# Performance work log

Measured on AMD Instinct MI355X. Metric: run time of the kernel, lower is better.

## Reference

```python
import jax, jax.numpy as jnp
import numpy as np

D_MODEL = 1024
H = 16
D_HEAD = D_MODEL // H
MASK_VAL = -1e30


def setup_inputs() -> dict:
    key = jax.random.key(0)
    ks = jax.random.split(key, 10)
    B, S = 2, 2048
    scale = 1.0 / np.sqrt(D_MODEL)
    return {
        "query": jax.random.normal(ks[0], (B, S, D_MODEL), jnp.float32),
        "key": jax.random.normal(ks[1], (B, S, D_MODEL), jnp.float32),
        "value": jax.random.normal(ks[2], (B, S, D_MODEL), jnp.float32),
        "mask": jax.random.randint(ks[3], (B, S, S), 0, 2) > 0,
        "Wq": jax.random.normal(ks[4], (D_MODEL, D_MODEL), jnp.float32) * scale,
        "bq": jnp.zeros((D_MODEL,), jnp.float32),
        "Wk": jax.random.normal(ks[5], (D_MODEL, D_MODEL), jnp.float32) * scale,
        "bk": jnp.zeros((D_MODEL,), jnp.float32),
        "Wv": jax.random.normal(ks[6], (D_MODEL, D_MODEL), jnp.float32) * scale,
        "bv": jnp.zeros((D_MODEL,), jnp.float32),
    }


def _split_heads(x, B, S):
    # [B,S,D] -> [B,H,S,Dh]
    return x.reshape(B, S, H, D_HEAD).transpose(0, 2, 1, 3)


def reference(query, key, value, mask, Wq, bq, Wk, bk, Wv, bv):
    B, S, _ = query.shape
    q = _split_heads(query @ Wq.T + bq, B, S)
    k = _split_heads(key @ Wk.T + bk, B, S)
    v = _split_heads(value @ Wv.T + bv, B, S)
    # scale by sqrt of per-head dim (query.size(-1) after split)
    q = q / jnp.sqrt(jnp.asarray(D_HEAD, q.dtype))
    scores = jnp.einsum("bhqd,bhkd->bhqk", q, k)
    scores = jnp.where(mask[:, None, :, :], MASK_VAL, scores)
    attn = jax.nn.softmax(scores, axis=-1)
    out = jnp.einsum("bhqk,bhkd->bhqd", attn, v)
    return out.transpose(0, 2, 1, 3).reshape(B, S, D_MODEL)
```

## Files before the change

kernel.cpp:

```cpp
#include <hip/hip_runtime.h>
#include <hip/hip_bf16.h>

#define D_MODEL 1024
#define NH 16
#define DH 64
#define S_LEN 2048
#define BATCH 2
#define QSCALE (0.125f * 1.44269504088896f)

#define KV_HSTRIDE (S_LEN * DH)
#define WS_V_OFF   (NH * KV_HSTRIDE)
#define KVB_WORDS  (2 * NH * KV_HSTRIDE)
#define MB_WORDS   ((S_LEN / 64) * S_LEN)
#define KTILE 128
#define NT (S_LEN / KTILE)
#define X_ELEMS (BATCH * S_LEN * D_MODEL)
#define W_ELEMS (D_MODEL * D_MODEL)
#define KSTR 88
#define VSTR 136
#define BUFW (128 * KSTR + 64 * VSTR)
#define BUF_BYTES (BUFW * 2)

typedef __attribute__((ext_vector_type(8))) short bf16x8;
typedef __attribute__((ext_vector_type(4))) float f32x4;
typedef __attribute__((ext_vector_type(2))) unsigned int u32x2;

static __device__ inline unsigned short f2bf(float f) {
    union { float f; unsigned u; } v; v.f = f;
    unsigned r = v.u + 0x7fffu + ((v.u >> 16) & 1u);
    return (unsigned short)(r >> 16);
}
static __device__ inline unsigned cvt2(float a, float b) {
    union { __hip_bfloat162 h2; unsigned u; } cv;
    cv.h2 = __float22bfloat162_rn(make_float2(a, b));
    return cv.u;
}
static __device__ inline bf16x8 pack8(f32x4 a, f32x4 b) {
    union { bf16x8 v; unsigned u[4]; } r;
    r.u[0] = cvt2(a[0], a[1]); r.u[1] = cvt2(a[2], a[3]);
    r.u[2] = cvt2(b[0], b[1]); r.u[3] = cvt2(b[2], b[3]);
    return r.v;
}
static __device__ inline bf16x8 cvt8(const float* __restrict__ p) {
    return pack8(*(const f32x4*)p, *(const f32x4*)(p + 4));
}
static __device__ inline float exp2_fast(float x) {
#if __has_builtin(__builtin_amdgcn_exp2f)
    return __builtin_amdgcn_exp2f(x);
#else
    return exp2f(x);
#endif
}
static __device__ inline void gload_lds16(const unsigned short* __restrict__ g,
                                          unsigned short* l, int lane) {
#if __has_builtin(__builtin_amdgcn_global_load_lds)
    __builtin_amdgcn_global_load_lds(
        (const __attribute__((address_space(1))) void*)g,
        (__attribute__((address_space(3))) void*)l, 16, 0, 0);
#else
    *(bf16x8*)((char*)l + lane * 16) = *(const bf16x8*)g;
#endif
}
static __device__ inline int vperm(int s) {
    return (s & ~31) | ((s & 12) << 1) | ((s & 16) >> 2) | (s & 3);
}

__global__ __launch_bounds__(256) void cvt_kernel(
    const float* __restrict__ q, const float* __restrict__ k,
    const float* __restrict__ v,
    const float* __restrict__ Wq, const float* __restrict__ Wk,
    const float* __restrict__ Wv,
    unsigned short* __restrict__ xb, unsigned short* __restrict__ wb)
{
    const int by = blockIdx.y;
    const float* src;
    unsigned short* dst;
    size_t base;
    if (blockIdx.x < 1024) {
        src = by == 0 ? q : (by == 1 ? k : v);
        dst = xb + (size_t)by * X_ELEMS;
        base = (size_t)blockIdx.x * 4096;
    } else {
        src = by == 0 ? Wq : (by == 1 ? Wk : Wv);
        dst = wb + (size_t)by * W_ELEMS;
        base = (size_t)(blockIdx.x - 1024) * 4096;
    }
    const int tid = threadIdx.x;
#pragma unroll
    for (int j = 0; j < 4; ++j) {
        const size_t o = base + (size_t)j * 1024 + (size_t)tid * 4;
        const f32x4 a = *(const f32x4*)(src + o);
        u32x2 r;
        r[0] = cvt2(a[0], a[1]);
        r[1] = cvt2(a[2], a[3]);
        *(u32x2*)&dst[o] = r;
    }
}

__global__ __launch_bounds__(256) void pack_mask_kernel(
    const int* __restrict__ mask, unsigned long long* __restrict__ mbits,
    int b_base)
{
    const int w    = blockIdx.x * 4 + (threadIdx.x >> 6);
    const int lane = threadIdx.x & 63;
    const int b    = b_base + (w >> 16);
    const int rem  = w & 65535;
    const int kt   = rem >> 11;
    const int s    = rem & 2047;
    const int v = mask[((size_t)b * S_LEN + s) * S_LEN + kt * 64 + lane];
    const unsigned long long bits = __ballot(v != 0);
    if (lane == 0) mbits[w] = bits;
}

__global__ __launch_bounds__(256) void proj_v2_kernel(
    const unsigned short* __restrict__ xb, const unsigned short* __restrict__ wb,
    const float* __restrict__ bq, const float* __restrict__ bk,
    const float* __restrict__ bv,
    float* __restrict__ q_out, unsigned short* __restrict__ ws)
{
    const int bx = blockIdx.x;
    const int by = blockIdx.y;
    const int z  = by >> 3;
    const int c0 = (by & 7) * 128;

    const unsigned short* A  = xb + (size_t)z * X_ELEMS;
    const unsigned short* Bw = wb + (size_t)z * W_ELEMS;
    const float* bias = z == 0 ? bq : (z == 1 ? bk : bv);

    const int tid  = threadIdx.x;
    const int wave = tid >> 6;
    const int lane = tid & 63;
    const int quad = lane >> 4;
    const int l16  = lane & 15;
    const int m0   = (wave & 1) * 64;
    const int n0   = (wave >> 1) * 64;

    __shared__ __align__(16) unsigned short As[128 * 32];
    __shared__ __align__(16) unsigned short Bs[128 * 32];

    const int r_lo = wave * 16 + (lane >> 2);
    const int r_hi = (wave + 4) * 16 + (lane >> 2);
    const int segu = (lane & 3) * 8;
    const int row0 = bx * 128;

    f32x4 acc[4][4] = {};

    for (int kk = 0; kk < D_MODEL; kk += 32) {
        gload_lds16(A  + (size_t)(row0 + r_lo) * D_MODEL + kk + segu, &As[wave * 512], lane);
        gload_lds16(A  + (size_t)(row0 + r_hi) * D_MODEL + kk + segu, &As[(wave + 4) * 512], lane);
        gload_lds16(Bw + (size_t)(c0 + r_lo) * D_MODEL + kk + segu, &Bs[wave * 512], lane);
        gload_lds16(Bw + (size_t)(c0 + r_hi) * D_MODEL + kk + segu, &Bs[(wave + 4) * 512], lane);
        __syncthreads();

        bf16x8 af[4], bfr[4];
#pragma unroll
        for (int i = 0; i < 4; ++i)
            af[i] = *(const bf16x8*)&As[(m0 + i * 16 + l16) * 32 + quad * 8];
#pragma unroll
        for (int j = 0; j < 4; ++j)
            bfr[j] = *(const bf16x8*)&Bs[(n0 + j * 16 + l16) * 32 + quad * 8];
#pragma unroll
        for (int i = 0; i < 4; ++i)
#pragma unroll
            for (int j = 0; j < 4; ++j)
                acc[i][j] = __builtin_amdgcn_mfma_f32_16x16x32_bf16(
                    af[i], bfr[j], acc[i][j], 0, 0, 0);
        __syncthreads();
    }

#pragma unroll
    for (int j = 0; j < 4; ++j) {
        const int cl  = c0 + n0 + j * 16 + l16;
        const float bval = bias[cl];
        const int h  = cl >> 6;
        const int dh = cl & 63;
#pragma unroll
        for (int i = 0; i < 4; ++i) {
#pragma unroll
            for (int r = 0; r < 4; ++r) {
                const int row = row0 + m0 + i * 16 + quad * 4 + r;
                const float v = acc[i][j][r] + bval;
                if (z == 0) {
                    q_out[(size_t)row * D_MODEL + cl] = v * QSCALE;
                } else {
                    unsigned short* slab = ws + (size_t)(row >> 11) * KVB_WORDS;
                    const int s = row & 2047;
                    if (z == 1)
                        slab[(size_t)h * KV_HSTRIDE + s * DH + dh] = f2bf(v);
                    else
                        slab[WS_V_OFF + (size_t)h * KV_HSTRIDE + dh * S_LEN + vperm(s)] = f2bf(v);
                }
            }
        }
    }
}

__global__ __launch_bounds__(256) void proj_fb_kernel(
    const float* __restrict__ q_in, const float* __restrict__ k_in,
    const float* __restrict__ v_in,
    const float* __restrict__ Wq, const float* __restrict__ bq,
    const float* __restrict__ Wk, const float* __restrict__ bk,
    const float* __restrict__ Wv, const float* __restrict__ bv,
    float* __restrict__ q_out, unsigned short* __restrict__ ws, int b_base)
{
    const int bx = blockIdx.x;
    const int by = blockIdx.y;
    const int z  = by >> 3;
    const int c0 = (by & 7) * 128;

    const float* x    = z == 0 ? q_in : (z == 1 ? k_in : v_in);
    const float* W    = z == 0 ? Wq   : (z == 1 ? Wk   : Wv);
    const float* bias = z == 0 ? bq   : (z == 1 ? bk   : bv);

    const int tid  = threadIdx.x;
    const int wave = tid >> 6;
    const int lane = tid & 63;
    const int quad = lane >> 4;
    const int l16  = lane & 15;
    const int m0   = (wave & 1) * 64;
    const int n0   = (wave >> 1) * 64;

    __shared__ __align__(16) unsigned short As[128][40];
    __shared__ __align__(16) unsigned short Bs[128][40];

    const int srow = tid >> 1;
    const int kcol = (tid & 1) * 16;
    const int row0 = b_base * S_LEN + bx * 128;
    const float* ag = x + (size_t)(row0 + srow) * D_MODEL + kcol;
    const float* bg = W + (size_t)(c0 + srow) * D_MODEL + kcol;

    f32x4 acc[4][4] = {};

    for (int kk = 0; kk < D_MODEL; kk += 32) {
        {
            f32x4 a0 = *(const f32x4*)(ag + kk);
            f32x4 a1 = *(const f32x4*)(ag + kk + 4);
            f32x4 a2 = *(const f32x4*)(ag + kk + 8);
            f32x4 a3 = *(const f32x4*)(ag + kk + 12);
            f32x4 b0 = *(const f32x4*)(bg + kk);
            f32x4 b1 = *(const f32x4*)(bg + kk + 4);
            f32x4 b2 = *(const f32x4*)(bg + kk + 8);
            f32x4 b3 = *(const f32x4*)(bg + kk + 12);
            *(bf16x8*)&As[srow][kcol]     = pack8(a0, a1);
            *(bf16x8*)&As[srow][kcol + 8] = pack8(a2, a3);
            *(bf16x8*)&Bs[srow][kcol]     = pack8(b0, b1);
            *(bf16x8*)&Bs[srow][kcol + 8] = pack8(b2, b3);
        }
        __syncthreads();

        bf16x8 af[4], bfr[4];
#pragma unroll
        for (int i = 0; i < 4; ++i)
            af[i] = *(const bf16x8*)&As[m0 + i * 16 + l16][quad * 8];
#pragma unroll
        for (int j = 0; j < 4; ++j)
            bfr[j] = *(const bf16x8*)&Bs[n0 + j * 16 + l16][quad * 8];
#pragma unroll
        for (int i = 0; i < 4; ++i)
#pragma unroll
            for (int j = 0; j < 4; ++j)
                acc[i][j] = __builtin_amdgcn_mfma_f32_16x16x32_bf16(
                    af[i], bfr[j], acc[i][j], 0, 0, 0);
        __syncthreads();
    }

#pragma unroll
    for (int j = 0; j < 4; ++j) {
        const int cl  = c0 + n0 + j * 16 + l16;
        const float bval = bias[cl];
        const int h  = cl >> 6;
        const int dh = cl & 63;
#pragma unroll
        for (int i = 0; i < 4; ++i) {
#pragma unroll
            for (int r = 0; r < 4; ++r) {
                const int row = row0 + m0 + i * 16 + quad * 4 + r;
                const float v = acc[i][j][r] + bval;
                if (z == 0) {
                    q_out[(size_t)row * D_MODEL + cl] = v * QSCALE;
                } else {
                    const int b_rel = (row >> 11) - b_base;
                    const int s     = row & 2047;
                    unsigned short* slab = ws + (size_t)b_rel * KVB_WORDS;
                    if (z == 1)
                        slab[(size_t)h * KV_HSTRIDE + s * DH + dh] = f2bf(v);
                    else
                        slab[WS_V_OFF + (size_t)h * KV_HSTRIDE + dh * S_LEN + vperm(s)] = f2bf(v);
                }
            }
        }
    }
}

__global__ __launch_bounds__(256) void attn_db_kernel(
    const unsigned short* __restrict__ ws,
    const unsigned long long* __restrict__ mbits,
    float* __restrict__ out)
{
    const int h     = blockIdx.x;
    const int qtile = blockIdx.y;
    const int bz    = blockIdx.z;

    const unsigned short* K  = ws + (size_t)bz * KVB_WORDS + (size_t)h * KV_HSTRIDE;
    const unsigned short* Vg = K + WS_V_OFF;
    const unsigned long long* mb = mbits + (size_t)bz * MB_WORDS;

    const int tid  = threadIdx.x;
    const int wave = tid >> 6;
    const int lane = tid & 63;
    const int quad = lane >> 4;
    const int l16  = lane & 15;
    const int q0   = qtile * 128;

    extern __shared__ __align__(16) unsigned short lds[];

    bf16x8 aq0a, aq1a, aq0b, aq1b;
    {
        const float* qa =
            out + (size_t)(bz * S_LEN + q0 + wave * 16 + l16) * D_MODEL + h * DH;
        const float* qb = qa + (size_t)64 * D_MODEL;
        aq0a = cvt8(qa + quad * 8);  aq1a = cvt8(qa + 32 + quad * 8);
        aq0b = cvt8(qb + quad * 8);  aq1b = cvt8(qb + 32 + quad * 8);
    }

    const int qg = q0 + wave * 16 + l16;
    float l_a = 0.f, l_b = 0.f;
    f32x4 o_a[4] = {}, o_b[4] = {};

    const int krow = tid >> 1, kc = (tid & 1) * 32;
    const int vrow = tid >> 2, vc = (tid & 3) * 32;
    bf16x8 kr[4], vr[4];
    {
        const unsigned short* kp = K + (size_t)krow * DH + kc;
        const unsigned short* vp = Vg + (size_t)vrow * S_LEN + vc;
#pragma unroll
        for (int i = 0; i < 4; ++i) {
            kr[i] = *(const bf16x8*)(kp + 8 * i);
            vr[i] = *(const bf16x8*)(vp + 8 * i);
        }
    }
    unsigned long long wm0a = mb[qg] >> (quad * 4);
    unsigned long long wm1a = mb[(size_t)S_LEN + qg] >> (quad * 4);
    unsigned long long wm0b = mb[qg + 64] >> (quad * 4);
    unsigned long long wm1b = mb[(size_t)S_LEN + qg + 64] >> (quad * 4);

    {
        unsigned short* Kt0 = lds;
        unsigned short* Vt0 = lds + 128 * KSTR;
#pragma unroll
        for (int i = 0; i < 4; ++i) {
            *(bf16x8*)&Kt0[krow * KSTR + kc + 8 * i] = kr[i];
            *(bf16x8*)&Vt0[vrow * VSTR + vc + 8 * i] = vr[i];
        }
    }

    for (int kt = 0; kt < NT; ++kt) {
        __syncthreads();
        unsigned short* Ktc = lds + (kt & 1) * BUFW;
        unsigned short* Vtc = Ktc + 128 * KSTR;

        if (kt + 1 < NT) {
            const unsigned short* kp = K + (size_t)((kt + 1) * KTILE + krow) * DH + kc;
            const unsigned short* vp = Vg + (size_t)vrow * S_LEN + (kt + 1) * KTILE + vc;
#pragma unroll
            for (int i = 0; i < 4; ++i) {
                kr[i] = *(const bf16x8*)(kp + 8 * i);
                vr[i] = *(const bf16x8*)(vp + 8 * i);
            }
        }
        unsigned long long nm0a = 0ull, nm1a = 0ull, nm0b = 0ull, nm1b = 0ull;
        if (kt + 1 < NT) {
            nm0a = mb[(size_t)(2 * kt + 2) * S_LEN + qg] >> (quad * 4);
            nm1a = mb[(size_t)(2 * kt + 3) * S_LEN + qg] >> (quad * 4);
            nm0b = mb[(size_t)(2 * kt + 2) * S_LEN + qg + 64] >> (quad * 4);
            nm1b = mb[(size_t)(2 * kt + 3) * S_LEN + qg + 64] >> (quad * 4);
        }

        bf16x8 af_a[4], af_b[4];
#pragma unroll
        for (int c = 0; c < 4; ++c) {
            f32x4 sa[2], sb[2];
            __builtin_amdgcn_s_setprio(1);
#pragma unroll
            for (int j = 0; j < 2; ++j) {
                const int blk = 2 * c + j;
                const unsigned short* kb = &Ktc[(blk * 16 + l16) * KSTR];
                bf16x8 k0 = *(const bf16x8*)&kb[quad * 8];
                bf16x8 k1 = *(const bf16x8*)&kb[32 + quad * 8];
                f32x4 z = {0.f, 0.f, 0.f, 0.f};
                sa[j] = __builtin_amdgcn_mfma_f32_16x16x32_bf16(k0, aq0a, z, 0, 0, 0);
                sa[j] = __builtin_amdgcn_mfma_f32_16x16x32_bf16(k1, aq1a, sa[j], 0, 0, 0);
                sb[j] = __builtin_amdgcn_mfma_f32_16x16x32_bf16(k0, aq0b, z, 0, 0, 0);
                sb[j] = __builtin_amdgcn_mfma_f32_16x16x32_bf16(k1, aq1b, sb[j], 0, 0, 0);
            }
            __builtin_amdgcn_s_setprio(0);
#pragma unroll
            for (int j = 0; j < 2; ++j) {
                const int blk = 2 * c + j;
                const unsigned long long wa = (blk < 4) ? wm0a : wm1a;
                const unsigned long long wb = (blk < 4) ? wm0b : wm1b;
                const int sh = (blk & 3) * 16;
#pragma unroll
                for (int r = 0; r < 4; ++r) {
                    const bool ma  = (wa >> (sh + r)) & 1ull;
                    const bool mbk = (wb >> (sh + r)) & 1ull;
                    const float pa = ma  ? 0.0f : exp2_fast(sa[j][r]);
                    const float pb = mbk ? 0.0f : exp2_fast(sb[j][r]);
                    sa[j][r] = pa; l_a += pa;
                    sb[j][r] = pb; l_b += pb;
                }
            }
            {
                union { bf16x8 v; unsigned u[4]; } pk;
                pk.u[0] = cvt2(sa[0][0], sa[0][1]);
                pk.u[1] = cvt2(sa[0][2], sa[0][3]);
                pk.u[2] = cvt2(sa[1][0], sa[1][1]);
                pk.u[3] = cvt2(sa[1][2], sa[1][3]);
                af_a[c] = pk.v;
                pk.u[0] = cvt2(sb[0][0], sb[0][1]);
                pk.u[1] = cvt2(sb[0][2], sb[0][3]);
                pk.u[2] = cvt2(sb[1][0], sb[1][1]);
                pk.u[3] = cvt2(sb[1][2], sb[1][3]);
                af_b[c] = pk.v;
            }
        }

        __builtin_amdgcn_s_setprio(1);
#pragma unroll
        for (int d = 0; d < 4; ++d) {
#pragma unroll
            for (int c = 0; c < 4; ++c) {
                bf16x8 bv = *(const bf16x8*)&Vtc[(d * 16 + l16) * VSTR + c * 32 + quad * 8];
                o_a[d] = __builtin_amdgcn_mfma_f32_16x16x32_bf16(af_a[c], bv, o_a[d], 0, 0, 0);
                o_b[d] = __builtin_amdgcn_mfma_f32_16x16x32_bf16(af_b[c], bv, o_b[d], 0, 0, 0);
            }
        }
        __builtin_amdgcn_s_setprio(0);

        if (kt + 1 < NT) {
            unsigned short* Ktn = lds + ((kt + 1) & 1) * BUFW;
            unsigned short* Vtn = Ktn + 128 * KSTR;
#pragma unroll
            for (int i = 0; i < 4; ++i) {
                *(bf16x8*)&Ktn[krow * KSTR + kc + 8 * i] = kr[i];
                *(bf16x8*)&Vtn[vrow * VSTR + vc + 8 * i] = vr[i];
            }
        }
        wm0a = nm0a; wm1a = nm1a; wm0b = nm0b; wm1b = nm1b;
    }

    l_a += __shfl_xor(l_a, 16, 64);
    l_a += __shfl_xor(l_a, 32, 64);
    l_b += __shfl_xor(l_b, 16, 64);
    l_b += __shfl_xor(l_b, 32, 64);

#pragma unroll
    for (int r = 0; r < 4; ++r) {
        const float la = __shfl(l_a, quad * 4 + r, 64);
        const float lb = __shfl(l_b, quad * 4 + r, 64);
        const float ia = 1.0f / fmaxf(la, 1e-30f);
        const float ib = 1.0f / fmaxf(lb, 1e-30f);
        const int qgr = q0 + wave * 16 + quad * 4 + r;
#pragma unroll
        for (int d = 0; d < 4; ++d) {
            out[((size_t)(bz * S_LEN) + qgr) * D_MODEL + h * DH + d * 16 + l16] =
                o_a[d][r] * ia;
            out[((size_t)(bz * S_LEN) + qgr + 64) * D_MODEL + h * DH + d * 16 + l16] =
                o_b[d][r] * ib;
        }
    }
}

__global__ __launch_bounds__(256) void attn_sb_kernel(
    const unsigned short* __restrict__ ws,
    const unsigned long long* __restrict__ mbits,
    const int* __restrict__ mask,
    float* __restrict__ out, int b_base, int use_bits)
{
    const int h     = blockIdx.x;
    const int qtile = blockIdx.y;
    const int bz    = blockIdx.z;
    const int b0    = b_base + bz;

    const unsigned short* K  = ws + (size_t)bz * KVB_WORDS + (size_t)h * KV_HSTRIDE;
    const unsigned short* Vg = K + WS_V_OFF;
    const unsigned long long* mb = mbits + (size_t)bz * MB_WORDS;

    const int tid  = threadIdx.x;
    const int wave = tid >> 6;
    const int lane = tid & 63;
    const int quad = lane >> 4;
    const int l16  = lane & 15;
    const int q0   = qtile * 128;

    __shared__ __align__(16) unsigned short Vt[64][VSTR];
    __shared__ __align__(16) unsigned short Kt[128 * KSTR];

    bf16x8 aq0a, aq1a, aq0b, aq1b;
    {
        const float* qa =
            out + (size_t)(b0 * S_LEN + q0 + wave * 16 + l16) * D_MODEL + h * DH;
        const float* qb = qa + (size_t)64 * D_MODEL;
        aq0a = cvt8(qa + quad * 8);  aq1a = cvt8(qa + 32 + quad * 8);
        aq0b = cvt8(qb + quad * 8);  aq1b = cvt8(qb + 32 + quad * 8);
    }

    const int qg = q0 + wave * 16 + l16;
    float l_a = 0.f, l_b = 0.f;
    f32x4 o_a[4] = {}, o_b[4] = {};

    const int krow = tid >> 1, kc = (tid & 1) * 32;
    const int vrow = tid >> 2, vc = (tid & 3) * 32;
    bf16x8 kr[4], vr[4];
    {
        const unsigned short* kp = K + (size_t)krow * DH + kc;
        const unsigned short* vp = Vg + (size_t)vrow * S_LEN + vc;
#pragma unroll
        for (int i = 0; i < 4; ++i) {
            kr[i] = *(const bf16x8*)(kp + 8 * i);
            vr[i] = *(const bf16x8*)(vp + 8 * i);
        }
    }

    for (int kt = 0; kt < NT; ++kt) {
#pragma unroll
        for (int i = 0; i < 4; ++i) {
            *(bf16x8*)&Kt[krow * KSTR + kc + 8 * i] = kr[i];
            *(bf16x8*)&Vt[vrow][vc + 8 * i]         = vr[i];
        }
        __syncthreads();

        if (kt + 1 < NT) {
            const unsigned short* kp = K + (size_t)((kt + 1) * KTILE + krow) * DH + kc;
            const unsigned short* vp = Vg + (size_t)vrow * S_LEN + (kt + 1) * KTILE + vc;
#pragma unroll
            for (int i = 0; i < 4; ++i) {
                kr[i] = *(const bf16x8*)(kp + 8 * i);
                vr[i] = *(const bf16x8*)(vp + 8 * i);
            }
        }

        unsigned long long wm0a = 0ull, wm1a = 0ull, wm0b = 0ull, wm1b = 0ull;
        if (use_bits) {
            wm0a = mb[(size_t)(2 * kt) * S_LEN + qg] >> (quad * 4);
            wm1a = mb[(size_t)(2 * kt + 1) * S_LEN + qg] >> (quad * 4);
            wm0b = mb[(size_t)(2 * kt) * S_LEN + qg + 64] >> (quad * 4);
            wm1b = mb[(size_t)(2 * kt + 1) * S_LEN + qg + 64] >> (quad * 4);
        }

        bf16x8 af_a[4], af_b[4];
#pragma unroll
        for (int c = 0; c < 4; ++c) {
            f32x4 sa[2], sb[2];
#pragma unroll
            for (int j = 0; j < 2; ++j) {
                const int blk = 2 * c + j;
                const unsigned short* kb = &Kt[(blk * 16 + l16) * KSTR];
                bf16x8 k0 = *(const bf16x8*)&kb[quad * 8];
                bf16x8 k1 = *(const bf16x8*)&kb[32 + quad * 8];
                f32x4 z = {0.f, 0.f, 0.f, 0.f};
                sa[j] = __builtin_amdgcn_mfma_f32_16x16x32_bf16(k0, aq0a, z, 0, 0, 0);
                sa[j] = __builtin_amdgcn_mfma_f32_16x16x32_bf16(k1, aq1a, sa[j], 0, 0, 0);
                sb[j] = __builtin_amdgcn_mfma_f32_16x16x32_bf16(k0, aq0b, z, 0, 0, 0);
                sb[j] = __builtin_amdgcn_mfma_f32_16x16x32_bf16(k1, aq1b, sb[j], 0, 0, 0);
            }
#pragma unroll
            for (int j = 0; j < 2; ++j) {
                const int blk = 2 * c + j;
                const unsigned long long wa = (blk < 4) ? wm0a : wm1a;
                const unsigned long long wb = (blk < 4) ? wm0b : wm1b;
                const int sh = (blk & 3) * 16;
#pragma unroll
                for (int r = 0; r < 4; ++r) {
                    bool ma, mbk;
                    if (use_bits) {
                        ma  = (wa >> (sh + r)) & 1ull;
                        mbk = (wb >> (sh + r)) & 1ull;
                    } else {
                        const int kg = kt * KTILE + blk * 16 + quad * 4 + r;
                        ma  = mask[((size_t)(b0 * S_LEN) + qg) * S_LEN + kg] != 0;
                        mbk = mask[((size_t)(b0 * S_LEN) + qg + 64) * S_LEN + kg] != 0;
                    }
                    const float pa = ma  ? 0.0f : exp2_fast(sa[j][r]);
                    const float pb = mbk ? 0.0f : exp2_fast(sb[j][r]);
                    sa[j][r] = pa; l_a += pa;
                    sb[j][r] = pb; l_b += pb;
                }
            }
            {
                union { bf16x8 v; unsigned u[4]; } pk;
                pk.u[0] = cvt2(sa[0][0], sa[0][1]);
                pk.u[1] = cvt2(sa[0][2], sa[0][3]);
                pk.u[2] = cvt2(sa[1][0], sa[1][1]);
                pk.u[3] = cvt2(sa[1][2], sa[1][3]);
                af_a[c] = pk.v;
                pk.u[0] = cvt2(sb[0][0], sb[0][1]);
                pk.u[1] = cvt2(sb[0][2], sb[0][3]);
                pk.u[2] = cvt2(sb[1][0], sb[1][1]);
                pk.u[3] = cvt2(sb[1][2], sb[1][3]);
                af_b[c] = pk.v;
            }
        }

#pragma unroll
        for (int d = 0; d < 4; ++d) {
#pragma unroll
            for (int c = 0; c < 4; ++c) {
                bf16x8 bv = *(const bf16x8*)&Vt[d * 16 + l16][c * 32 + quad * 8];
                o_a[d] = __builtin_amdgcn_mfma_f32_16x16x32_bf16(af_a[c], bv, o_a[d], 0, 0, 0);
                o_b[d] = __builtin_amdgcn_mfma_f32_16x16x32_bf16(af_b[c], bv, o_b[d], 0, 0, 0);
            }
        }
        __syncthreads();
    }

    l_a += __shfl_xor(l_a, 16, 64);
    l_a += __shfl_xor(l_a, 32, 64);
    l_b += __shfl_xor(l_b, 16, 64);
    l_b += __shfl_xor(l_b, 32, 64);

#pragma unroll
    for (int r = 0; r < 4; ++r) {
        const float la = __shfl(l_a, quad * 4 + r, 64);
        const float lb = __shfl(l_b, quad * 4 + r, 64);
        const float ia = 1.0f / fmaxf(la, 1e-30f);
        const float ib = 1.0f / fmaxf(lb, 1e-30f);
        const int qgr = q0 + wave * 16 + quad * 4 + r;
#pragma unroll
        for (int d = 0; d < 4; ++d) {
            out[((size_t)(b0 * S_LEN) + qgr) * D_MODEL + h * DH + d * 16 + l16] =
                o_a[d][r] * ia;
            out[((size_t)(b0 * S_LEN) + qgr + 64) * D_MODEL + h * DH + d * 16 + l16] =
                o_b[d][r] * ib;
        }
    }
}

extern "C" void kernel_launch(void* const* d_in, const int* in_sizes, int n_in,
                              void* d_out, int out_size, void* d_ws, size_t ws_size,
                              hipStream_t stream) {
    const float* query = (const float*)d_in[0];
    const float* key   = (const float*)d_in[1];
    const float* value = (const float*)d_in[2];
    const int*   mask  = (const int*)d_in[3];
    const float* Wq    = (const float*)d_in[4];
    const float* bq    = (const float*)d_in[5];
    const float* Wk    = (const float*)d_in[6];
    const float* bk    = (const float*)d_in[7];
    const float* Wv    = (const float*)d_in[8];
    const float* bv    = (const float*)d_in[9];

    unsigned short* ws   = (unsigned short*)d_ws;
    float*          outp = (float*)d_out;

    const size_t KV_BYTES = (size_t)KVB_WORDS * 2;
    const size_t MB_BYTES = (size_t)MB_WORDS * 8;
    const size_t XB_BYTES = (size_t)3 * X_ELEMS * 2;
    const size_t WB_BYTES = (size_t)3 * W_ELEMS * 2;
    const size_t base2    = 2 * KV_BYTES + 2 * MB_BYTES;

    static int db_ok = -1;
    if (db_ok < 0) {
        hipError_t e = hipFuncSetAttribute(
            reinterpret_cast<const void*>(attn_db_kernel),
            hipFuncAttributeMaxDynamicSharedMemorySize, 2 * BUF_BYTES);
        db_ok = (e == hipSuccess) ? 1 : 0;
    }

    if (ws_size >= base2 + XB_BYTES + WB_BYTES) {
        unsigned long long* mbits = (unsigned long long*)(ws + 2 * KVB_WORDS);
        unsigned short* xb = ws + base2 / 2;
        unsigned short* wb = xb + (size_t)3 * X_ELEMS;
        cvt_kernel<<<dim3(1280, 3), 256, 0, stream>>>(
            query, key, value, Wq, Wk, Wv, xb, wb);
        proj_v2_kernel<<<dim3(32, 24), 256, 0, stream>>>(
            xb, wb, bq, bk, bv, outp, ws);
        pack_mask_kernel<<<dim3(2 * MB_WORDS / 4), 256, 0, stream>>>(mask, mbits, 0);
        if (db_ok)
            attn_db_kernel<<<dim3(NH, S_LEN / 128, 2), 256, 2 * BUF_BYTES, stream>>>(
                ws, mbits, outp);
        else
            attn_sb_kernel<<<dim3(NH, S_LEN / 128, 2), 256, 0, stream>>>(
                ws, mbits, mask, outp, 0, 1);
    } else if (ws_size >= base2) {
        unsigned long long* mbits = (unsigned long long*)(ws + 2 * KVB_WORDS);
        proj_fb_kernel<<<dim3(32, 24), 256, 0, stream>>>(
            query, key, value, Wq, bq, Wk, bk, Wv, bv, outp, ws, 0);
        pack_mask_kernel<<<dim3(2 * MB_WORDS / 4), 256, 0, stream>>>(mask, mbits, 0);
        if (db_ok)
            attn_db_kernel<<<dim3(NH, S_LEN / 128, 2), 256, 2 * BUF_BYTES, stream>>>(
                ws, mbits, outp);
        else
            attn_sb_kernel<<<dim3(NH, S_LEN / 128, 2), 256, 0, stream>>>(
                ws, mbits, mask, outp, 0, 1);
    } else if (ws_size >= KV_BYTES + MB_BYTES) {
        unsigned long long* mbits = (unsigned long long*)(ws + KVB_WORDS);
        for (int b0 = 0; b0 < BATCH; ++b0) {
            proj_fb_kernel<<<dim3(16, 24), 256, 0, stream>>>(
                query, key, value, Wq, bq, Wk, bk, Wv, bv, outp, ws, b0);
            pack_mask_kernel<<<dim3(MB_WORDS / 4), 256, 0, stream>>>(mask, mbits, b0);
            attn_sb_kernel<<<dim3(NH, S_LEN / 128, 1), 256, 0, stream>>>(
                ws, mbits, mask, outp, b0, 1);
        }
    } else {
        for (int b0 = 0; b0 < BATCH; ++b0) {
            proj_fb_kernel<<<dim3(16, 24), 256, 0, stream>>>(
                query, key, value, Wq, bq, Wk, bk, Wv, bv, outp, ws, b0);
            attn_sb_kernel<<<dim3(NH, S_LEN / 128, 1), 256, 0, stream>>>(
                ws, (const unsigned long long*)ws, mask, outp, b0, 0);
        }
    }
}
```

Baseline: 251.9 us.

## Fuse mask packing into conversion kernel and transpose V output through LDS

Mask bit-packing now runs inside the fp32-to-bf16 conversion kernel as extra blocks, so one fewer kernel launch is needed and the two memory-bound jobs share the GPU. Separately, the V-projection epilogue stages tiles in a shared-memory transpose buffer and writes 16-byte vectors to the transposed/permuted V layout, replacing scattered 2-byte stores. The price is extra LDS use and more barriers in the projection kernel, which may lower occupancy.

```diff
diff --git a/kernel.cpp b/kernel.cpp
--- a/kernel.cpp
+++ b/kernel.cpp
@@ -65,35 +65,56 @@
     return (s & ~31) | ((s & 12) << 1) | ((s & 16) >> 2) | (s & 3);
 }
 
-__global__ __launch_bounds__(256) void cvt_kernel(
+__global__ __launch_bounds__(256) void cvtpack_kernel(
     const float* __restrict__ q, const float* __restrict__ k,
     const float* __restrict__ v,
     const float* __restrict__ Wq, const float* __restrict__ Wk,
     const float* __restrict__ Wv,
-    unsigned short* __restrict__ xb, unsigned short* __restrict__ wb)
+    unsigned short* __restrict__ xb, unsigned short* __restrict__ wb,
+    const int* __restrict__ mask, unsigned long long* __restrict__ mbits)
 {
-    const int by = blockIdx.y;
-    const float* src;
-    unsigned short* dst;
-    size_t base;
-    if (blockIdx.x < 1024) {
-        src = by == 0 ? q : (by == 1 ? k : v);
-        dst = xb + (size_t)by * X_ELEMS;
-        base = (size_t)blockIdx.x * 4096;
+    const int bid = blockIdx.x;
+    if (bid < 3840) {
+        const int z = bid / 1280;
+        const int rr = bid - z * 1280;
+        const float* src;
+        unsigned short* dst;
+        size_t base;
+        if (rr < 1024) {
+            src = z == 0 ? q : (z == 1 ? k : v);
+            dst = xb + (size_t)z * X_ELEMS;
+            base = (size_t)rr * 4096;
+        } else {
+            src = z == 0 ? Wq : (z == 1 ? Wk : Wv);
+            dst = wb + (size_t)z * W_ELEMS;
+            base = (size_t)(rr - 1024) * 4096;
+        }
+        const int tid = threadIdx.x;
+#pragma unroll
+        for (int j = 0; j < 4; ++j) {
+            const size_t o = base + (size_t)j * 1024 + (size_t)tid * 4;
+            const f32x4 a = *(const f32x4*)(src + o);
+            u32x2 r;
+            r[0] = cvt2(a[0], a[1]);
+            r[1] = cvt2(a[2], a[3]);
+            *(u32x2*)&dst[o] = r;
+        }
     } else {
-        src = by == 0 ? Wq : (by == 1 ? Wk : Wv);
-        dst = wb + (size_t)by * W_ELEMS;
-        base = (size_t)(blockIdx.x - 1024) * 4096;
-    }
-    const int tid = threadIdx.x;
-#pragma unroll
-    for (int j = 0; j < 4; ++j) {
-        const size_t o = base + (size_t)j * 1024 + (size_t)tid * 4;
-        const f32x4 a = *(const f32x4*)(src + o);
-        u32x2 r;
-        r[0] = cvt2(a[0], a[1]);
-        r[1] = cvt2(a[2], a[3]);
-        *(u32x2*)&dst[o] = r;
+        const int pb   = bid - 3840;
+        const int wave = threadIdx.x >> 6;
+        const int lane = threadIdx.x & 63;
+        const int w0   = pb * 16 + wave * 4;
+#pragma unroll
+        for (int j = 0; j < 4; ++j) {
+            const int w   = w0 + j;
+            const int b   = w >> 16;
+            const int rem = w & 65535;
+            const int kt  = rem >> 11;
+            const int s   = rem & 2047;
+            const int vm  = mask[((size_t)b * S_LEN + s) * S_LEN + kt * 64 + lane];
+            const unsigned long long bits = __ballot(vm != 0);
+            if (lane == 0) mbits[w] = bits;
+        }
     }
 }
 
@@ -137,6 +158,7 @@
 
     __shared__ __align__(16) unsigned short As[128 * 32];
     __shared__ __align__(16) unsigned short Bs[128 * 32];
+    __shared__ __align__(16) unsigned short Tt[64][136];
 
     const int r_lo = wave * 16 + (lane >> 2);
     const int r_hi = (wave + 4) * 16 + (lane >> 2);
@@ -168,28 +190,63 @@
         __syncthreads();
     }
 
-#pragma unroll
-    for (int j = 0; j < 4; ++j) {
-        const int cl  = c0 + n0 + j * 16 + l16;
-        const float bval = bias[cl];
-        const int h  = cl >> 6;
-        const int dh = cl & 63;
-#pragma unroll
-        for (int i = 0; i < 4; ++i) {
-#pragma unroll
-            for (int r = 0; r < 4; ++r) {
-                const int row = row0 + m0 + i * 16 + quad * 4 + r;
-                const float v = acc[i][j][r] + bval;
-                if (z == 0) {
-                    q_out[(size_t)row * D_MODEL + cl] = v * QSCALE;
-                } else {
-                    unsigned short* slab = ws + (size_t)(row >> 11) * KVB_WORDS;
-                    const int s = row & 2047;
-                    if (z == 1)
+    if (z != 2) {
+#pragma unroll
+        for (int j = 0; j < 4; ++j) {
+            const int cl  = c0 + n0 + j * 16 + l16;
+            const float bval = bias[cl];
+            const int h  = cl >> 6;
+            const int dh = cl & 63;
+#pragma unroll
+            for (int i = 0; i < 4; ++i) {
+#pragma unroll
+                for (int r = 0; r < 4; ++r) {
+                    const int row = row0 + m0 + i * 16 + quad * 4 + r;
+                    const float v = acc[i][j][r] + bval;
+                    if (z == 0) {
+                        q_out[(size_t)row * D_MODEL + cl] = v * QSCALE;
+                    } else {
+                        unsigned short* slab = ws + (size_t)(row >> 11) * KVB_WORDS;
+                        const int s = row & 2047;
                         slab[(size_t)h * KV_HSTRIDE + s * DH + dh] = f2bf(v);
-                    else
-                        slab[WS_V_OFF + (size_t)h * KV_HSTRIDE + dh * S_LEN + vperm(s)] = f2bf(v);
+                    }
                 }
+            }
+        }
+    } else {
+        unsigned short* slab = ws + (size_t)(row0 >> 11) * KVB_WORDS;
+        const int s_base = row0 & 2047;
+#pragma unroll
+        for (int p = 0; p < 2; ++p) {
+            __syncthreads();
+            if ((wave >> 1) == p) {
+#pragma unroll
+                for (int j = 0; j < 4; ++j) {
+                    const int col_local = j * 16 + l16;
+                    const float bval = bias[c0 + n0 + j * 16 + l16];
+#pragma unroll
+                    for (int i = 0; i < 4; ++i) {
+                        const int sbase = m0 + i * 16 + quad * 4;
+                        const int k5 = sbase & 31;
+                        const int dst = (sbase & ~31) | (((k5 & 12) << 1) | ((k5 & 16) >> 2));
+                        u32x2 w;
+                        w[0] = cvt2(acc[i][j][0] + bval, acc[i][j][1] + bval);
+                        w[1] = cvt2(acc[i][j][2] + bval, acc[i][j][3] + bval);
+                        *(u32x2*)&Tt[col_local][dst] = w;
+                    }
+                }
+            }
+            __syncthreads();
+            const int row_ = tid >> 2;
+            const int cl2  = c0 + p * 64 + row_;
+            const int h2   = cl2 >> 6;
+            const int dh2  = cl2 & 63;
+            unsigned short* drow =
+                slab + WS_V_OFF + (size_t)h2 * KV_HSTRIDE + (size_t)dh2 * S_LEN + s_base;
+#pragma unroll
+            for (int cc = 0; cc < 4; ++cc) {
+                const int s_off = cc * 32 + (tid & 3) * 8;
+                *(bf16x8*)&drow[s_off] = *(const bf16x8*)&Tt[row_][s_off];
             }
         }
     }
@@ -671,11 +728,10 @@
         unsigned long long* mbits = (unsigned long long*)(ws + 2 * KVB_WORDS);
         unsigned short* xb = ws + base2 / 2;
         unsigned short* wb = xb + (size_t)3 * X_ELEMS;
-        cvt_kernel<<<dim3(1280, 3), 256, 0, stream>>>(
-            query, key, value, Wq, Wk, Wv, xb, wb);
+        cvtpack_kernel<<<dim3(3840 + 8192), 256, 0, stream>>>(
+            query, key, value, Wq, Wk, Wv, xb, wb, mask, mbits);
         proj_v2_kernel<<<dim3(32, 24), 256, 0, stream>>>(
             xb, wb, bq, bk, bv, outp, ws);
-        pack_mask_kernel<<<dim3(2 * MB_WORDS / 4), 256, 0, stream>>>(mask, mbits, 0);
         if (db_ok)
             attn_db_kernel<<<dim3(NH, S_LEN / 128, 2), 256, 2 * BUF_BYTES, stream>>>(
                 ws, mbits, outp);
```

Result: no change. 254.0 us (+0.8%).
